# Performance work log

Hardware: AMD Instinct MI355X
Metric: run time of the kernel (lower is better)

## Reference

```python
import jax, jax.numpy as jnp
import numpy as np
import math

H = 32       # num_attention_heads
HKV = 8      # num_key_value_heads
D = 128      # attention_head_size


def setup_inputs() -> dict:
    key = jax.random.key(0)
    k1, k2, k3 = jax.random.split(key, 3)
    B, L = 2, 2048
    return {
        "query_states": jax.random.normal(k1, (B, L, H * D), dtype=jnp.float32),
        "key_states": jax.random.normal(k2, (B, L, HKV * D), dtype=jnp.float32),
        "value_states": jax.random.normal(k3, (B, L, HKV * D), dtype=jnp.float32),
    }


def reference(query_states, key_states, value_states):
    B, L, _ = query_states.shape
    groups = H // HKV

    # view + transpose(1,2): (B, heads, L, D)
    q = query_states.reshape(B, L, H, D).transpose(0, 2, 1, 3)
    k = key_states.reshape(B, L, HKV, D).transpose(0, 2, 1, 3)
    v = value_states.reshape(B, L, HKV, D).transpose(0, 2, 1, 3)

    # repeat_kv: repeat_interleave along head dim
    k = jnp.repeat(k, groups, axis=1)
    v = jnp.repeat(v, groups, axis=1)

    q = q.astype(jnp.float16)
    k = k.astype(jnp.float16)
    v = v.astype(jnp.float16)

    # source: transpose(1,2) -> (B, L, H, D), then reshape(B*H, L, D)
    # (row-major reshape of the (B,L,H,D) layout, replicated exactly)
    q = q.transpose(0, 2, 1, 3).reshape(B * H, L, D)
    k = k.transpose(0, 2, 1, 3).reshape(B * H, L, D)
    v = v.transpose(0, 2, 1, 3).reshape(B * H, L, D)

    scale = 1.0 / math.sqrt(D)
    attn_scores = jnp.einsum("bqd,bkd->bqk", q, k) * jnp.float16(scale)
    attn_weights = jax.nn.softmax(attn_scores, axis=-1)
    attn_output = jnp.einsum("bqk,bkd->bqd", attn_weights, v)

    # reshape(B,H,L,D).transpose(1,2) -> (B,L,H,D) -> (B, L, H*D)
    attn_output = attn_output.reshape(B, H, L, D).transpose(0, 2, 1, 3)
    return attn_output.reshape(B, L, H * D)
```

## Files before the change

kernel.cpp:

```cpp
#include <hip/hip_runtime.h>
#include <hip/hip_bf16.h>

typedef _Float16 f16;
typedef f16 f16x2 __attribute__((ext_vector_type(2)));
typedef f16 f16x4 __attribute__((ext_vector_type(4)));
typedef f16 f16x8 __attribute__((ext_vector_type(8)));
typedef float f32x4 __attribute__((ext_vector_type(4)));

#define NB   2
#define LL   2048
#define LQ   2048
#define LKV  512
#define DD   128
#define BM   128
#define BN   64
#define KS_STR 132
#define VT_STR 68
#define PT_STR 68

__global__ __launch_bounds__(256, 2)
void fa_fwd(const float* __restrict__ qg,
            const float* __restrict__ kg,
            const float* __restrict__ vg,
            float* __restrict__ og)
{
    __shared__ __align__(16) f16 smem[BN*KS_STR + DD*VT_STR + BM*PT_STR];
    f16* Ks = smem;
    f16* Vt = smem + BN*KS_STR;
    f16* Pt = smem + BN*KS_STR + DD*VT_STR;

    const int tid  = threadIdx.x;
    const int wave = tid >> 6;
    const int lane = tid & 63;
    const int ln   = lane & 15;
    const int qd   = lane >> 4;

    const int qt   = blockIdx.x;
    const int g    = blockIdx.y;
    const int bb   = g >> 5;
    const int lhi  = g & 31;

    const float* qmat = qg + (size_t)(bb*LL + 64*lhi)*4096;
    const float* kmat = kg + (size_t)(bb*LL + 64*lhi)*1024;
    const float* vmat = vg + (size_t)(bb*LL + 64*lhi)*1024;

    const int qbase = qt*BM + wave*32;

    f16x8 qf[2][4];
#pragma unroll
    for (int nt = 0; nt < 2; ++nt) {
        const float* qrow = qmat + (size_t)(qbase + 16*nt + ln)*DD;
#pragma unroll
        for (int kc = 0; kc < 4; ++kc) {
            const float4* qp = (const float4*)(qrow + kc*32 + 8*qd);
            float4 f0 = qp[0], f1 = qp[1];
            f16x8 t = { (f16)f0.x,(f16)f0.y,(f16)f0.z,(f16)f0.w,
                        (f16)f1.x,(f16)f1.y,(f16)f1.z,(f16)f1.w };
            qf[nt][kc] = t;
        }
    }

    f32x4 o[2][8];
#pragma unroll
    for (int nt = 0; nt < 2; ++nt)
#pragma unroll
        for (int dmt = 0; dmt < 8; ++dmt)
#pragma unroll
            for (int r = 0; r < 4; ++r) o[nt][dmt][r] = 0.0f;

    float mrun[2] = {-1e30f, -1e30f}, lrun[2] = {0.0f, 0.0f};
    const float SC2 = 0.08837890625f * 1.44269504088896340f;

    for (int kt = 0; kt < LKV/BN; ++kt) {
        const float* kb = kmat + kt*BN*DD;
        const float* vb = vmat + kt*BN*DD;

#pragma unroll
        for (int i = 0; i < 8; ++i) {
            int f = tid + i*256;
            int row = f >> 5, c4 = f & 31;
            float4 x = *(const float4*)(kb + f*4);
            f16x4 h4 = { (f16)x.x,(f16)x.y,(f16)x.z,(f16)x.w };
            *(f16x4*)(Ks + row*KS_STR + c4*4) = h4;
        }
#pragma unroll
        for (int i = 0; i < 8; ++i) {
            int f = tid + i*256;
            int kvr = f & 63, c4 = f >> 6;
            float4 x = *(const float4*)(vb + (size_t)kvr*DD + c4*4);
            Vt[(c4*4+0)*VT_STR + kvr] = (f16)x.x;
            Vt[(c4*4+1)*VT_STR + kvr] = (f16)x.y;
            Vt[(c4*4+2)*VT_STR + kvr] = (f16)x.z;
            Vt[(c4*4+3)*VT_STR + kvr] = (f16)x.w;
        }
        __syncthreads();

        f32x4 st[2][4];
#pragma unroll
        for (int nt = 0; nt < 2; ++nt)
#pragma unroll
            for (int mt = 0; mt < 4; ++mt)
#pragma unroll
                for (int r = 0; r < 4; ++r) st[nt][mt][r] = 0.0f;
#pragma unroll
        for (int mt = 0; mt < 4; ++mt) {
            const f16* kr = Ks + (16*mt + ln)*KS_STR + 8*qd;
#pragma unroll
            for (int kc = 0; kc < 4; ++kc) {
                f16x4 a0 = *(const f16x4*)(kr + kc*32);
                f16x4 a1 = *(const f16x4*)(kr + kc*32 + 4);
                f16x8 af = __builtin_shufflevector(a0, a1, 0,1,2,3,4,5,6,7);
#pragma unroll
                for (int nt = 0; nt < 2; ++nt)
                    st[nt][mt] = __builtin_amdgcn_mfma_f32_16x16x32_f16(af, qf[nt][kc], st[nt][mt], 0,0,0);
            }
        }

        float alph[2];
#pragma unroll
        for (int nt = 0; nt < 2; ++nt) {
            float mx = -1e30f;
#pragma unroll
            for (int mt = 0; mt < 4; ++mt)
#pragma unroll
                for (int r = 0; r < 4; ++r) {
                    float v = st[nt][mt][r]*SC2; st[nt][mt][r] = v; mx = fmaxf(mx, v);
                }
            mx = fmaxf(mx, __shfl_xor(mx, 16, 64));
            mx = fmaxf(mx, __shfl_xor(mx, 32, 64));
            float mnew = fmaxf(mrun[nt], mx);
            alph[nt] = exp2f(mrun[nt] - mnew);
            float rs = 0.0f;
#pragma unroll
            for (int mt = 0; mt < 4; ++mt)
#pragma unroll
                for (int r = 0; r < 4; ++r) {
                    float p = exp2f(st[nt][mt][r] - mnew);
                    st[nt][mt][r] = p; rs += p;
                }
            rs += __shfl_xor(rs, 16, 64);
            rs += __shfl_xor(rs, 32, 64);
            lrun[nt] = lrun[nt]*alph[nt] + rs;
            mrun[nt] = mnew;
        }

#pragma unroll
        for (int nt = 0; nt < 2; ++nt) {
            f16* prow = Pt + (wave*32 + 16*nt + ln)*PT_STR + 4*qd;
#pragma unroll
            for (int mt = 0; mt < 4; ++mt)
#pragma unroll
                for (int p2 = 0; p2 < 2; ++p2) {
                    f16x2 pp = { (f16)st[nt][mt][2*p2], (f16)st[nt][mt][2*p2+1] };
                    *(f16x2*)(prow + 16*mt + 2*p2) = pp;
                }
        }

#pragma unroll
        for (int nt = 0; nt < 2; ++nt)
#pragma unroll
            for (int dmt = 0; dmt < 8; ++dmt)
#pragma unroll
                for (int r = 0; r < 4; ++r) o[nt][dmt][r] *= alph[nt];

#pragma unroll
        for (int kc2 = 0; kc2 < 2; ++kc2) {
            f16x8 pf[2];
#pragma unroll
            for (int nt = 0; nt < 2; ++nt) {
                const f16* pr = Pt + (wave*32 + 16*nt + ln)*PT_STR + kc2*32 + 8*qd;
                f16x4 b0 = *(const f16x4*)(pr);
                f16x4 b1 = *(const f16x4*)(pr + 4);
                pf[nt] = __builtin_shufflevector(b0, b1, 0,1,2,3,4,5,6,7);
            }
#pragma unroll
            for (int dmt = 0; dmt < 8; ++dmt) {
                const f16* vr = Vt + (16*dmt + ln)*VT_STR + kc2*32 + 8*qd;
                f16x4 a0 = *(const f16x4*)(vr);
                f16x4 a1 = *(const f16x4*)(vr + 4);
                f16x8 vf = __builtin_shufflevector(a0, a1, 0,1,2,3,4,5,6,7);
#pragma unroll
                for (int nt = 0; nt < 2; ++nt)
                    o[nt][dmt] = __builtin_amdgcn_mfma_f32_16x16x32_f16(vf, pf[nt], o[nt][dmt], 0,0,0);
            }
        }
        __syncthreads();
    }

#pragma unroll
    for (int nt = 0; nt < 2; ++nt) {
        float inv = 1.0f / lrun[nt];
        int qtok = qbase + 16*nt + ln;
        float* orow = og + (size_t)(bb*LL + qtok)*4096 + lhi*DD + 4*qd;
#pragma unroll
        for (int dmt = 0; dmt < 8; ++dmt) {
            float4 x = { o[nt][dmt][0]*inv, o[nt][dmt][1]*inv,
                         o[nt][dmt][2]*inv, o[nt][dmt][3]*inv };
            *(float4*)(orow + 16*dmt) = x;
        }
    }
}

extern "C" void kernel_launch(void* const* d_in, const int* in_sizes, int n_in,
                              void* d_out, int out_size, void* d_ws, size_t ws_size,
                              hipStream_t stream) {
    (void)in_sizes; (void)n_in; (void)out_size; (void)d_ws; (void)ws_size;
    const float* q = (const float*)d_in[0];
    const float* k = (const float*)d_in[1];
    const float* v = (const float*)d_in[2];
    float* o = (float*)d_out;
    dim3 grid(LQ/BM, 64, 1), block(256);
    hipLaunchKernelGGL(fa_fwd, grid, block, 0, stream, q, k, v, o);
}
```

Measured before the change: 215.3 us.

## Prepack K/V to swizzled fp16 workspace and async-load tiles into LDS

Adds a prepack kernel that converts K and V to fp16 once per call, writing K row-major and V transposed, both with an XOR swizzle, into the workspace. The attention kernel then loads each tile with global_load_lds directly into LDS, prefetching the next K and V tiles while computing on the current ones. This replaces the repeated per-block fp32 loads, conversion and scattered transpose. It also remaps block IDs so blocks sharing a head group land close together for L2 reuse, and raises the occupancy target to 3 blocks per CU. The cost is an extra kernel launch, a workspace round-trip, and a fallback path kept for when no workspace is provided.

```diff
diff --git a/kernel.cpp b/kernel.cpp
--- a/kernel.cpp
+++ b/kernel.cpp
@@ -1,5 +1,4 @@
 #include <hip/hip_runtime.h>
-#include <hip/hip_bf16.h>
 
 typedef _Float16 f16;
 typedef f16 f16x2 __attribute__((ext_vector_type(2)));
@@ -14,15 +13,248 @@
 #define DD   128
 #define BM   128
 #define BN   64
+#define NKT  (LKV/BN)
+#define PT_STR 68
 #define KS_STR 132
 #define VT_STR 68
-#define PT_STR 68
+
+#define G_STRIDE 65536ull
+#define WS_BYTES (2ull*64ull*G_STRIDE*2ull)
+
+#define GLOAD16(gsrc, ldst) \
+    __builtin_amdgcn_global_load_lds((const __attribute__((address_space(1))) void*)(gsrc), \
+                                     (__attribute__((address_space(3))) void*)(ldst), 16, 0, 0)
+
+__global__ __launch_bounds__(256)
+void prepack(const float* __restrict__ kg, const float* __restrict__ vg,
+             f16* __restrict__ ws)
+{
+    __shared__ float vtile[64*132];
+    const int tid = threadIdx.x;
+    const int kt  = blockIdx.x;
+    const int g   = blockIdx.y;
+
+    if (blockIdx.z == 0) {
+        const float* kb = kg + (size_t)g*65536 + (size_t)kt*8192;
+        f16* kout = ws + (size_t)g*G_STRIDE + (size_t)kt*8192;
+#pragma unroll
+        for (int i = 0; i < 4; ++i) {
+            int q = i*256 + tid;
+            int r = q >> 4, c = q & 15;
+            const float* src = kb + r*128 + ((c ^ (r&7))*8);
+            float4 a = *(const float4*)src;
+            float4 b = *(const float4*)(src + 4);
+            f16x8 h = { (f16)a.x,(f16)a.y,(f16)a.z,(f16)a.w,
+                        (f16)b.x,(f16)b.y,(f16)b.z,(f16)b.w };
+            *(f16x8*)(kout + (size_t)q*8) = h;
+        }
+    } else {
+        const float* vb = vg + (size_t)g*65536 + (size_t)kt*8192;
+        f16* vout = ws + 64ull*G_STRIDE + (size_t)g*G_STRIDE + (size_t)kt*8192;
+#pragma unroll
+        for (int i = 0; i < 8; ++i) {
+            int f = tid + i*256;
+            int row = f >> 5, c4 = f & 31;
+            float4 x = *(const float4*)(vb + (size_t)f*4);
+            *(float4*)(vtile + row*132 + c4*4) = x;
+        }
+        __syncthreads();
+#pragma unroll
+        for (int i = 0; i < 4; ++i) {
+            int q = i*256 + tid;
+            int r = q >> 3, c = q & 7;
+            int kv0 = (c ^ (r&7))*8;
+            f16x8 h;
+#pragma unroll
+            for (int j = 0; j < 8; ++j) h[j] = (f16)vtile[(kv0+j)*132 + r];
+            *(f16x8*)(vout + (size_t)q*8) = h;
+        }
+    }
+}
+
+__global__ __launch_bounds__(256, 3)
+void fa_fwd(const float* __restrict__ qg, const f16* __restrict__ ws,
+            float* __restrict__ og)
+{
+    __shared__ __align__(16) f16 Ks[BN*DD];
+    __shared__ __align__(16) f16 Vt[DD*BN];
+    __shared__ __align__(16) f16 Pt[BM*PT_STR];
+
+    const int tid  = threadIdx.x;
+    const int wave = tid >> 6;
+    const int lane = tid & 63;
+    const int ln   = lane & 15;
+    const int qd   = lane >> 4;
+
+    const int bid = blockIdx.x;
+    const int qt  = (bid >> 3) & 15;
+    const int g   = ((bid & 7) << 3) | (bid >> 7);
+    const int bb  = g >> 5;
+    const int lhi = g & 31;
+
+    const float* qmat = qg + (size_t)(bb*LL + 64*lhi)*4096;
+    const f16*   kw   = ws + (size_t)g*G_STRIDE;
+    const f16*   vw   = ws + (64ull + (size_t)g)*G_STRIDE;
+
+    const int qbase = qt*BM + wave*32;
+
+    auto issueK = [&](int kt) {
+#pragma unroll
+        for (int i = 0; i < 4; ++i)
+            GLOAD16(kw + (size_t)kt*8192 + (size_t)(i*256 + tid)*8,
+                    Ks + (i*256 + wave*64)*8);
+    };
+    auto issueV = [&](int kt) {
+#pragma unroll
+        for (int i = 0; i < 4; ++i)
+            GLOAD16(vw + (size_t)kt*8192 + (size_t)(i*256 + tid)*8,
+                    Vt + (i*256 + wave*64)*8);
+    };
+
+    issueK(0);
+    issueV(0);
+
+    f16x8 qf[2][4];
+#pragma unroll
+    for (int nt = 0; nt < 2; ++nt) {
+        const float* qrow = qmat + (size_t)(qbase + 16*nt + ln)*DD;
+#pragma unroll
+        for (int kc = 0; kc < 4; ++kc) {
+            const float4* qp = (const float4*)(qrow + kc*32 + 8*qd);
+            float4 f0 = qp[0], f1 = qp[1];
+            f16x8 t = { (f16)f0.x,(f16)f0.y,(f16)f0.z,(f16)f0.w,
+                        (f16)f1.x,(f16)f1.y,(f16)f1.z,(f16)f1.w };
+            qf[nt][kc] = t;
+        }
+    }
+
+    f32x4 o[2][8];
+#pragma unroll
+    for (int nt = 0; nt < 2; ++nt)
+#pragma unroll
+        for (int dmt = 0; dmt < 8; ++dmt)
+#pragma unroll
+            for (int r = 0; r < 4; ++r) o[nt][dmt][r] = 0.0f;
+
+    float mrun[2] = {-1e30f, -1e30f}, lrun[2] = {0.0f, 0.0f};
+    const float SC2 = 0.08837890625f * 1.44269504088896340f;
+
+    __syncthreads();
+
+#pragma unroll 1
+    for (int t = 0; t < NKT; ++t) {
+        f32x4 st[2][4];
+#pragma unroll
+        for (int nt = 0; nt < 2; ++nt)
+#pragma unroll
+            for (int mt = 0; mt < 4; ++mt)
+#pragma unroll
+                for (int r = 0; r < 4; ++r) st[nt][mt][r] = 0.0f;
+#pragma unroll
+        for (int mt = 0; mt < 4; ++mt) {
+            const int R = 16*mt + ln;
+#pragma unroll
+            for (int kc = 0; kc < 4; ++kc) {
+                f16x8 af = *(const f16x8*)(Ks + R*DD + (((kc*4 + qd) ^ (R&7))*8));
+#pragma unroll
+                for (int nt = 0; nt < 2; ++nt)
+                    st[nt][mt] = __builtin_amdgcn_mfma_f32_16x16x32_f16(af, qf[nt][kc], st[nt][mt], 0,0,0);
+            }
+        }
+
+        float alph[2];
+#pragma unroll
+        for (int nt = 0; nt < 2; ++nt) {
+            float mx = -1e30f;
+#pragma unroll
+            for (int mt = 0; mt < 4; ++mt)
+#pragma unroll
+                for (int r = 0; r < 4; ++r) {
+                    float v = st[nt][mt][r]*SC2; st[nt][mt][r] = v; mx = fmaxf(mx, v);
+                }
+            mx = fmaxf(mx, __shfl_xor(mx, 16, 64));
+            mx = fmaxf(mx, __shfl_xor(mx, 32, 64));
+            float mnew = fmaxf(mrun[nt], mx);
+            alph[nt] = exp2f(mrun[nt] - mnew);
+            float rs = 0.0f;
+#pragma unroll
+            for (int mt = 0; mt < 4; ++mt)
+#pragma unroll
+                for (int r = 0; r < 4; ++r) {
+                    float p = exp2f(st[nt][mt][r] - mnew);
+                    st[nt][mt][r] = p; rs += p;
+                }
+            rs += __shfl_xor(rs, 16, 64);
+            rs += __shfl_xor(rs, 32, 64);
+            lrun[nt] = lrun[nt]*alph[nt] + rs;
+            mrun[nt] = mnew;
+        }
+
+#pragma unroll
+        for (int nt = 0; nt < 2; ++nt) {
+            f16* prow = Pt + (wave*32 + 16*nt + ln)*PT_STR + 4*qd;
+#pragma unroll
+            for (int mt = 0; mt < 4; ++mt)
+#pragma unroll
+                for (int p2 = 0; p2 < 2; ++p2) {
+                    f16x2 pp = { (f16)st[nt][mt][2*p2], (f16)st[nt][mt][2*p2+1] };
+                    *(f16x2*)(prow + 16*mt + 2*p2) = pp;
+                }
+        }
+
+        __syncthreads();
+        if (t+1 < NKT) issueK(t+1);
+
+#pragma unroll
+        for (int nt = 0; nt < 2; ++nt)
+#pragma unroll
+            for (int dmt = 0; dmt < 8; ++dmt)
+#pragma unroll
+                for (int r = 0; r < 4; ++r) o[nt][dmt][r] *= alph[nt];
+
+#pragma unroll
+        for (int kc2 = 0; kc2 < 2; ++kc2) {
+            f16x8 pf[2];
+#pragma unroll
+            for (int nt = 0; nt < 2; ++nt) {
+                const f16* pr = Pt + (wave*32 + 16*nt + ln)*PT_STR + kc2*32 + 8*qd;
+                f16x4 b0 = *(const f16x4*)(pr);
+                f16x4 b1 = *(const f16x4*)(pr + 4);
+                pf[nt] = __builtin_shufflevector(b0, b1, 0,1,2,3,4,5,6,7);
+            }
+#pragma unroll
+            for (int dmt = 0; dmt < 8; ++dmt) {
+                const int R = 16*dmt + ln;
+                f16x8 vf = *(const f16x8*)(Vt + R*BN + (((kc2*4 + qd) ^ (R&7))*8));
+#pragma unroll
+                for (int nt = 0; nt < 2; ++nt)
+                    o[nt][dmt] = __builtin_amdgcn_mfma_f32_16x16x32_f16(vf, pf[nt], o[nt][dmt], 0,0,0);
+            }
+        }
+
+        __syncthreads();
+        if (t+1 < NKT) issueV(t+1);
+    }
+
+#pragma unroll
+    for (int nt = 0; nt < 2; ++nt) {
+        float inv = 1.0f / lrun[nt];
+        int qtok = qbase + 16*nt + ln;
+        float* orow = og + (size_t)(bb*LL + qtok)*4096 + lhi*DD + 4*qd;
+#pragma unroll
+        for (int dmt = 0; dmt < 8; ++dmt) {
+            float4 x = { o[nt][dmt][0]*inv, o[nt][dmt][1]*inv,
+                         o[nt][dmt][2]*inv, o[nt][dmt][3]*inv };
+            *(float4*)(orow + 16*dmt) = x;
+        }
+    }
+}
 
 __global__ __launch_bounds__(256, 2)
-void fa_fwd(const float* __restrict__ qg,
-            const float* __restrict__ kg,
-            const float* __restrict__ vg,
-            float* __restrict__ og)
+void fa_fwd_fb(const float* __restrict__ qg,
+               const float* __restrict__ kg,
+               const float* __restrict__ vg,
+               float* __restrict__ og)
 {
     __shared__ __align__(16) f16 smem[BN*KS_STR + DD*VT_STR + BM*PT_STR];
     f16* Ks = smem;
@@ -204,11 +436,18 @@
 extern "C" void kernel_launch(void* const* d_in, const int* in_sizes, int n_in,
                               void* d_out, int out_size, void* d_ws, size_t ws_size,
                               hipStream_t stream) {
-    (void)in_sizes; (void)n_in; (void)out_size; (void)d_ws; (void)ws_size;
+    (void)in_sizes; (void)n_in; (void)out_size;
     const float* q = (const float*)d_in[0];
     const float* k = (const float*)d_in[1];
     const float* v = (const float*)d_in[2];
     float* o = (float*)d_out;
-    dim3 grid(LQ/BM, 64, 1), block(256);
-    hipLaunchKernelGGL(fa_fwd, grid, block, 0, stream, q, k, v, o);
+    if (d_ws != nullptr && ws_size >= (size_t)WS_BYTES) {
+        hipLaunchKernelGGL(prepack, dim3(8, 64, 2), dim3(256), 0, stream,
+                           k, v, (f16*)d_ws);
+        hipLaunchKernelGGL(fa_fwd, dim3(1024), dim3(256), 0, stream,
+                           q, (const f16*)d_ws, o);
+    } else {
+        hipLaunchKernelGGL(fa_fwd_fb, dim3(LQ/BM, 64), dim3(256), 0, stream,
+                           q, k, v, o);
+    }
 }
```

New measurement: 218.0 us. Within noise of the previous version (+1.3%).
